# Performance work log

Hardware: AMD Instinct MI355X
Metric: run time of the kernel (lower is better)

## Reference

```python
import jax, jax.numpy as jnp
import numpy as np
import math

N_QUBITS = 10
N_VQC_LAYERS = 3
N_ACTIONS = 3
B = 4096
T = 128
D = 1 << N_QUBITS
IU, JU = np.triu_indices(N_QUBITS, 1)  # combinations(range(N),2) order


def _ry(a):
    # [B] (or scalar) -> [...,2,2] complex64 RY(a)
    c, s = jnp.cos(a * 0.5), jnp.sin(a * 0.5)
    return jnp.stack([jnp.stack([c, -s], -1), jnp.stack([s, c], -1)], -2).astype(jnp.complex64)


def _rz(a):
    h = a.astype(jnp.complex64) * 0.5
    z = jnp.zeros_like(h)
    return jnp.stack([jnp.stack([jnp.exp(-1j * h), z], -1), jnp.stack([z, jnp.exp(1j * h)], -1)], -2)


def _rot(w):
    # Rot(phi,theta,omega) = RZ(omega) @ RY(theta) @ RZ(phi); w=[phi,theta,omega]
    return _rz(w[2]) @ _ry(w[1]) @ _rz(w[0])


def _apply_1q(state, gate, q, n):
    # apply 2x2 gate to qubit q of [B, 2^n] state (bit q has stride 2^(n-q-1))
    b, d = state.shape
    lo = 1 << (n - q - 1)
    hi = 1 << q
    s = state.reshape(b, hi, 2, lo)
    if gate.ndim == 3:
        s = jnp.einsum('bij,bhjl->bhil', gate, s)
    else:
        s = jnp.einsum('ij,bhjl->bhil', gate, s)
    return s.reshape(b, d)


def _static_tables(n, n_layers):
    s = np.arange(1 << n)
    # IsingZZ sign masks: +1 if bits differ, -1 if equal (matches torch buffer)
    masks = np.stack([
        np.where(((s >> (n - 1 - qi)) & 1) ^ ((s >> (n - 1 - qj)) & 1) == 1, 1.0, -1.0)
        for qi, qj in zip(IU, JU)
    ]).astype(np.float32)
    # PauliZ expectation signs per qubit
    zsigns = np.where(((s[None, :] >> (n - 1 - np.arange(n)[:, None])) & 1) == 0, 1.0, -1.0).astype(np.float32)
    # CNOT ring as index permutations (same math as the dense matmul in torch)
    perms = []
    for l in range(n_layers):
        rng = l % (n - 1) + 1 if n > 1 else 1
        layer = []
        for ctrl in range(n):
            tgt = (ctrl + rng) % n
            cb = (s >> (n - 1 - ctrl)) & 1
            layer.append(np.where(cb == 1, s ^ (1 << (n - 1 - tgt)), s))
        perms.append(layer)
    return masks, zsigns, perms


MASKS, ZSIGNS, PERMS = _static_tables(N_QUBITS, N_VQC_LAYERS)


def setup_inputs() -> dict:
    key = jax.random.key(0)
    k1, k2, k3, k4 = jax.random.split(key, 4)
    return {
        'c_kt': jax.random.normal(k1, (B, T, N_QUBITS), jnp.float32),
        'delta_c_kt': jax.random.normal(k2, (B, T, N_QUBITS), jnp.float32),
        'vqc_weights': jax.random.normal(k3, (N_VQC_LAYERS, N_QUBITS, 3), jnp.float32),
        'w_proj': jax.random.normal(k4, (N_ACTIONS, N_QUBITS), jnp.float32) / math.sqrt(N_QUBITS),
        'b_proj': jnp.zeros((N_ACTIONS,), jnp.float32),
        'log_alpha': jnp.zeros((), jnp.float32),
    }


def reference(c_kt, delta_c_kt, vqc_weights, w_proj, b_proj, log_alpha):
    n, L = N_QUBITS, N_VQC_LAYERS
    b, t, k_ = c_kt.shape
    # --- IsingCouplingEstimator: Pearson corr -> tanh(rho * alpha), zero diag ---
    feat = c_kt + 0.5 * delta_c_kt
    X = jnp.swapaxes(feat, 1, 2)                      # [B, K, T]
    Xc = X - X.mean(-1, keepdims=True)
    std = jnp.maximum(jnp.sqrt((Xc * Xc).sum(-1, keepdims=True) / (t - 1)), 1e-8)
    Xn = Xc / std
    rho = jnp.einsum('bit,bjt->bij', Xn, Xn) / (t - 1)
    rho = rho * (1.0 - jnp.eye(k_, dtype=rho.dtype))
    J = jnp.tanh(rho * jnp.exp(log_alpha))            # [B, K, K]
    j_upper = J[:, IU, JU]                            # [B, K*(K-1)/2]

    # --- angle encoding from last timestep ---
    theta = c_kt[:, -1, :]                            # [B, K]
    phi = delta_c_kt[:, -1, :]

    # --- TorchVQC state-vector simulation ---
    state = jnp.zeros((b, D), jnp.complex64).at[:, 0].set(1.0 + 0j)
    for q in range(n):
        state = _apply_1q(state, _ry(theta[:, q]), q, n)
        state = _apply_1q(state, _rz(phi[:, q]), q, n)
    # all IsingZZ phases fused: exp(0.5j * pi * sum_p J_p * mask_p)
    ang = math.pi * (j_upper @ jnp.asarray(MASKS))    # [B, D]
    state = state * jnp.exp(0.5j * ang.astype(jnp.complex64))
    for l in range(L):
        for q in range(n):
            state = _apply_1q(state, _rot(vqc_weights[l, q]), q, n)
        for q in range(n):
            state = state[:, PERMS[l][q]]             # CNOT as permutation
        if l < L - 1:                                 # data re-uploading
            for q in range(n):
                state = _apply_1q(state, _ry(theta[:, q] * 0.5), q, n)
                state = _apply_1q(state, _rz(phi[:, q] * 0.5), q, n)
    probs = jnp.real(state) ** 2 + jnp.imag(state) ** 2
    expvals = probs @ jnp.asarray(ZSIGNS).T           # [B, N] <Z_k>

    # --- logit projection ---
    return expvals @ w_proj.T + b_proj                # [B, n_actions]
```

## Files before the change

### kernel.cpp

```cpp
#include <hip/hip_runtime.h>


typedef float v2 __attribute__((ext_vector_type(2)));

struct M10 { unsigned row[10]; };
constexpr M10 mident() { M10 m{}; for (int i=0;i<10;++i) m.row[i]=1u<<i; return m; }
constexpr M10 mmul(M10 A, M10 B) {
  M10 C{};
  for (int i=0;i<10;++i){ unsigned x=0; for (int j=0;j<10;++j) if ((A.row[i]>>j)&1u) x ^= B.row[j]; C.row[i]=x; }
  return C;
}
constexpr M10 cnotT(int ctrl, int rng) {
  const int tgt = (ctrl + rng) % 10;
  const int cb = 9 - ctrl, tb = 9 - tgt;
  M10 m = mident(); m.row[tb] = (1u<<tb)|(1u<<cb); return m;
}
constexpr M10 blockPinv(int rng) { M10 m = cnotT(0,rng); for (int c=1;c<10;++c) m = mmul(m, cnotT(c,rng)); return m; }
constexpr M10 blockP(int rng)    { M10 m = cnotT(9,rng); for (int c=8;c>=0;--c) m = mmul(m, cnotT(c,rng)); return m; }
constexpr unsigned mcol(M10 A, int c) { unsigned x=0; for (int i=0;i<10;++i) x |= ((A.row[i]>>c)&1u)<<i; return x; }
constexpr int par(unsigned x){ int p=0; for (int i=0;i<10;++i) p ^= (int)((x>>i)&1u); return p; }
constexpr int topbit4(int x){ int b=0; for (int i=1;i<4;++i) if (x>>i) b=i; return 1<<b; }

constexpr M10 Q1  = blockP(1);
constexpr M10 Q1i = blockPinv(1);
constexpr M10 Q2  = mmul(blockP(2), Q1);
constexpr M10 Q2i = mmul(Q1i, blockPinv(2));
constexpr M10 Q3  = mmul(blockP(3), Q2);

static_assert(mmul(Q1, Q1i).row[0]==1u && mmul(Q1,Q1i).row[9]==(1u<<9), "inv1");
static_assert(mmul(Q2, Q2i).row[0]==1u && mmul(Q2,Q2i).row[7]==(1u<<7), "inv2");
static_assert(par(mcol(Q1i,0)&Q1.row[0]) && par(mcol(Q1i,5)&Q1.row[5]) && par(mcol(Q1i,9)&Q1.row[9]), "dual1");
static_assert(par(mcol(Q2i,0)&Q2.row[0]) && par(mcol(Q2i,4)&Q2.row[4]) && par(mcol(Q2i,9)&Q2.row[9]), "dual2");

template<int CTRL>
__device__ __forceinline__ float dppf(float v) {
  return __int_as_float(__builtin_amdgcn_update_dpp(
      0, __float_as_int(v), CTRL, 0xF, 0xF, true));
}

template<int MASK>
__device__ __forceinline__ float xany(float v, int baddr) {
  constexpr int QC[4] = {0, 0xB1, 0x4E, 0x1B};
  if constexpr (MASK == 0) return v;
  else if constexpr (MASK <= 3) return dppf<QC[MASK]>(v);
  else if constexpr (MASK == 4) return dppf<0x141>(dppf<0x1B>(v));
  else if constexpr (MASK == 8) return dppf<0x128>(v);
  else if constexpr (MASK >= 9 && MASK <= 11) return dppf<QC[MASK&3]>(dppf<0x128>(v));
  else if constexpr (MASK < 32) return __int_as_float(__builtin_amdgcn_ds_swizzle(__float_as_int(v), (MASK<<10)|0x1F));
  else return __int_as_float(__builtin_amdgcn_ds_bpermute(baddr, __float_as_int(v)));
}
template<int MASK>
__device__ __forceinline__ v2 xany2(v2 v, int baddr) {
  v2 r; r.x = xany<MASK>(v.x, baddr); r.y = xany<MASK>(v.y, baddr); return r;
}

template<int LM>
__device__ __forceinline__ float xshfl(float v) {
  if constexpr (LM == 1) return dppf<0xB1>(v);
  else if constexpr (LM == 2) return dppf<0x4E>(v);
  else if constexpr (LM == 4) return dppf<0x141>(dppf<0x1B>(v));
  else if constexpr (LM == 8) return dppf<0x128>(v);
  else if constexpr (LM == 16) return __int_as_float(__builtin_amdgcn_ds_swizzle(__float_as_int(v), 0x401F));
  else return __shfl_xor(v, 32);
}

template<int B, int NP>
__device__ __forceinline__ void fstage(float* p, int lane) {
  #pragma unroll
  for (int i = 0; i < NP; ++i) {
    const float send = (lane & B) ? p[i] : p[i + NP];
    const float recv = xshfl<B>(send);
    const float keep = (lane & B) ? p[i + NP] : p[i];
    p[i] = keep + recv;
  }
}
constexpr int holder_lane45(int v) {
  const int a = v >= 24; int r = v - 24 * a;
  const int b = r >= 12; r -= 12 * b;
  const int c = r >= 6;  r -= 6 * c;
  const int d = r >= 3;  r -= 3 * d;
  const int e = r >= 2;  r -= 2 * e;
  return a | (b << 1) | (c << 2) | (d << 3) | (e << 4) | (r << 5);
}
constexpr int holder_lane10(int v) {
  const int a = v >= 5; int r = v - 5 * a;
  const int b = r >= 3; r -= 3 * b;
  const int c = r >= 2; r -= 2 * c;
  return a | (b << 1) | (c << 2) | (r << 3);
}

__device__ __forceinline__ float rfl(float x) {
  return __int_as_float(__builtin_amdgcn_readfirstlane(__float_as_int(x)));
}
#define RLg(g_, x_) __int_as_float(__builtin_amdgcn_readlane(__float_as_int(x_), (g_)))

__device__ __forceinline__ float fast_tanh(float x) {
  return 1.0f - 2.0f / (__expf(2.0f * x) + 1.0f);
}
__device__ __forceinline__ v2 sneg(v2 a) {
  v2 r; r.x = -a.y; r.y = a.x; return r;
}

template<int M, int V>
__device__ __forceinline__ void gate_g(v2 (&st)[16], int lane,
                                       float ar, float ai, float br, float bi) {
  constexpr int MR = M & 15, ML = (M >> 4) & 63;
  constexpr int VR = V & 15, VL = (V >> 4) & 63;
  bool hl = false;
  if constexpr (VL != 0) hl = (__builtin_popcount(lane & VL) & 1) != 0;
  const float aiX = hl ? -ai : ai;
  const float brX = hl ? -br : br;
  int baddr = 0;
  if constexpr (ML >= 32) baddr = (lane ^ ML) << 2;
  if constexpr (MR == 0) {
    #pragma unroll
    for (int r = 0; r < 16; ++r) {
      const v2 p = xany2<ML>(st[r], baddr);
      const v2 a = st[r];
      if ((__builtin_popcount(r & VR) & 1) == 0)
        st[r] = ar*a + aiX*sneg(a) + brX*p + bi*sneg(p);
      else
        st[r] = ar*a - aiX*sneg(a) - brX*p + bi*sneg(p);
    }
  } else {
    constexpr int HB = topbit4(MR);
    #pragma unroll
    for (int r = 0; r < 16; ++r) {
      if ((r & HB) == 0) {
        const int r1 = r ^ MR;
        v2 pa, pb;
        if constexpr (ML == 0) { pa = st[r1]; pb = st[r]; }
        else { pa = xany2<ML>(st[r1], baddr); pb = xany2<ML>(st[r], baddr); }
        const v2 a = st[r], b = st[r1];
        if ((__builtin_popcount(r & VR) & 1) == 0)
          st[r] = ar*a + aiX*sneg(a) + brX*pa + bi*sneg(pa);
        else
          st[r] = ar*a - aiX*sneg(a) - brX*pa + bi*sneg(pa);
        if ((__builtin_popcount(r1 & VR) & 1) == 0)
          st[r1] = ar*b + aiX*sneg(b) + brX*pb + bi*sneg(pb);
        else
          st[r1] = ar*b - aiX*sneg(b) - brX*pb + bi*sneg(pb);
      }
    }
  }
}

template<int I, int J>
__device__ __forceinline__ void pair_accum(float t, int lane, float& Cc,
                                           float (&dcf)[4], float (&ecf)[6]) {
  if constexpr (J <= 5) {
    const bool diff = (((lane >> (5 - I)) ^ (lane >> (5 - J))) & 1) != 0;
    Cc += diff ? -t : t;
  } else if constexpr (I <= 5) {
    const bool b = ((lane >> (5 - I)) & 1) != 0;
    dcf[J - 6] += b ? -t : t;
  } else {
    constexpr int eb = (I == 6) ? 0 : (I == 7) ? 3 : 5;
    ecf[eb + (J - I - 1)] = t;
  }
}
#define PACC(v_, i_, j_) pair_accum<i_, j_>(RLg(holder_lane45(v_), tl), lane, Cc, dcoef, ecoef);

#define GATE0(g_, q_) gate_g<(1<<(9-(q_))), (1<<(9-(q_)))>(st, lane, \
    RLg(g_,Mr00), RLg(g_,Mi00), RLg(g_,Mr01), RLg(g_,Mi01));
#define GATE1(g_, q_) gate_g<(int)mcol(Q1i,9-(q_)), (int)Q1.row[9-(q_)]>(st, lane, \
    RLg(g_,Mr00), RLg(g_,Mi00), RLg(g_,Mr01), RLg(g_,Mi01));
#define GATE2(g_, q_) gate_g<(int)mcol(Q2i,9-(q_)), (int)Q2.row[9-(q_)]>(st, lane, \
    RLg(g_,Mr00), RLg(g_,Mi00), RLg(g_,Mr01), RLg(g_,Mi01));

extern "C" __global__ void __launch_bounds__(256, 2)
qhl_kernel(const float* __restrict__ c_kt, const float* __restrict__ dc_kt,
           const float* __restrict__ vw,  const float* __restrict__ w_proj,
           const float* __restrict__ b_proj, const float* __restrict__ log_alpha,
           float* __restrict__ out) {
  const int wave = threadIdx.x >> 6;
  const int lane = threadIdx.x & 63;
  const int bid  = blockIdx.x * 4 + wave;

  const float* c   = c_kt  + (size_t)bid * 1280;
  const float* dcp = dc_kt + (size_t)bid * 1280;

  float Mr00, Mi00, Mr01, Mi01;
  {
    const int g = lane < 30 ? lane : 0;
    const int l = g / 10, q = g - l * 10;
    const float w0 = vw[g*3+0], w1 = vw[g*3+1], w2 = vw[g*3+2];
    float cY, sY; __sincosf(0.5f*w1, &sY, &cY);
    float ca, sa; __sincosf(0.5f*(w0+w2), &sa, &ca);
    float cb, sb; __sincosf(0.5f*(w0-w2), &sb, &cb);
    const float r00r =  cY*ca, r00i = -cY*sa, r01r = -sY*cb, r01i = -sY*sb;
    if (l == 0) {
      Mr00 = r00r; Mi00 = r00i; Mr01 = r01r; Mi01 = r01i;
    } else {
      const float thq = c[1270 + q], phq = dcp[1270 + q];
      float cy, sy; __sincosf(0.25f * thq, &sy, &cy);
      float cz, sz; __sincosf(0.25f * phq, &sz, &cz);
      const float e00r =  cy*cz, e00i = -cy*sz, e01r = -sy*cz, e01i =  sy*sz;
      const float e10r =  sy*cz, e10i =  sy*sz, e11r =  cy*cz, e11i =  cy*sz;
      Mr00 = r00r*e00r - r00i*e00i + r01r*e10r - r01i*e10i;
      Mi00 = r00r*e00i + r00i*e00r + r01r*e10i + r01i*e10r;
      Mr01 = r00r*e01r - r00i*e01i + r01r*e11r - r01i*e11i;
      Mi01 = r00r*e01i + r00i*e01r + r01r*e11i + r01i*e11r;
    }
  }

  v2 ym[10];
  {
    const float2* c0 = (const float2*)(c   + lane * 10);
    const float2* d0 = (const float2*)(dcp + lane * 10);
    const float2* c1 = (const float2*)(c   + (lane + 64) * 10);
    const float2* d1 = (const float2*)(dcp + (lane + 64) * 10);
    #pragma unroll
    for (int k = 0; k < 5; ++k) {
      const float2 a0 = c0[k], b0 = d0[k], a1 = c1[k], b1 = d1[k];
      ym[2*k].x   = a0.x + 0.5f * b0.x;  ym[2*k].y   = a1.x + 0.5f * b1.x;
      ym[2*k+1].x = a0.y + 0.5f * b0.y;  ym[2*k+1].y = a1.y + 0.5f * b1.y;
    }
  }

  {
    float mb[6];
    float m10a[10];
    #pragma unroll
    for (int k = 0; k < 10; ++k) m10a[k] = ym[k].x + ym[k].y;
    #pragma unroll
    for (int i = 0; i < 5; ++i) {
      const float send = (lane & 1) ? m10a[i] : m10a[i + 5];
      const float recv = xshfl<1>(send);
      const float keep = (lane & 1) ? m10a[i + 5] : m10a[i];
      mb[i] = keep + recv;
    }
    mb[5] = 0.0f;
    fstage<2, 3>(mb, lane);
    mb[3] = 0.0f;
    fstage<4, 2>(mb, lane);
    fstage<8, 1>(mb, lane);
    mb[0] += xshfl<16>(mb[0]);
    mb[0] += xshfl<32>(mb[0]);
    mb[0] *= (1.0f / 128.0f);
    #pragma unroll
    for (int k = 0; k < 10; ++k) {
      const float mk = RLg(holder_lane10(k), mb[0]);
      ym[k].x -= mk; ym[k].y -= mk;
    }
    float s10[10];
    #pragma unroll
    for (int k = 0; k < 10; ++k) { const v2 sq = ym[k] * ym[k]; s10[k] = sq.x + sq.y; }
    #pragma unroll
    for (int i = 0; i < 5; ++i) {
      const float send = (lane & 1) ? s10[i] : s10[i + 5];
      const float recv = xshfl<1>(send);
      const float keep = (lane & 1) ? s10[i + 5] : s10[i];
      mb[i] = keep + recv;
    }
    mb[5] = 0.0f;
    fstage<2, 3>(mb, lane);
    mb[3] = 0.0f;
    fstage<4, 2>(mb, lane);
    fstage<8, 1>(mb, lane);
    mb[0] += xshfl<16>(mb[0]);
    mb[0] += xshfl<32>(mb[0]);
    const float rsv = fminf(__builtin_amdgcn_rsqf(mb[0] * (1.0f / 127.0f)), 1e8f);
    #pragma unroll
    for (int k = 0; k < 10; ++k) {
      const float rk = RLg(holder_lane10(k), rsv);
      ym[k].x *= rk; ym[k].y *= rk;
    }
  }

  const float expA = rfl(__expf(log_alpha[0]));
  float Cc = 0.0f, dcoef[4] = {0, 0, 0, 0}, ecoef[6];
  float tl;
  {
    constexpr int PI_[45] = {0,0,0,0,0,0,0,0,0, 1,1,1,1,1,1,1,1, 2,2,2,2,2,2,2,
                             3,3,3,3,3,3, 4,4,4,4,4, 5,5,5,5, 6,6,6, 7,7, 8};
    constexpr int PJ_[45] = {1,2,3,4,5,6,7,8,9, 2,3,4,5,6,7,8,9, 3,4,5,6,7,8,9,
                             4,5,6,7,8,9, 5,6,7,8,9, 6,7,8,9, 7,8,9, 8,9, 9};
    float p[48];
    #pragma unroll
    for (int v = 0; v < 45; ++v) {
      const v2 pr = ym[PI_[v]] * ym[PJ_[v]];
      p[v] = pr.x + pr.y;
    }
    p[45] = 0.0f; p[46] = 0.0f; p[47] = 0.0f;
    fstage<1, 24>(p, lane);
    fstage<2, 12>(p, lane);
    fstage<4, 6>(p, lane);
    fstage<8, 3>(p, lane);
    p[3] = 0.0f;
    fstage<16, 2>(p, lane);
    fstage<32, 1>(p, lane);
    const float sc = expA * (1.0f / 127.0f);
    tl = -1.5707963267948966f * fast_tanh(p[0] * sc);
  }
  PACC(0,0,1) PACC(1,0,2) PACC(2,0,3) PACC(3,0,4) PACC(4,0,5) PACC(5,0,6) PACC(6,0,7) PACC(7,0,8) PACC(8,0,9)
  PACC(9,1,2) PACC(10,1,3) PACC(11,1,4) PACC(12,1,5) PACC(13,1,6) PACC(14,1,7) PACC(15,1,8) PACC(16,1,9)
  PACC(17,2,3) PACC(18,2,4) PACC(19,2,5) PACC(20,2,6) PACC(21,2,7) PACC(22,2,8) PACC(23,2,9)
  PACC(24,3,4) PACC(25,3,5) PACC(26,3,6) PACC(27,3,7) PACC(28,3,8) PACC(29,3,9)
  PACC(30,4,5) PACC(31,4,6) PACC(32,4,7) PACC(33,4,8) PACC(34,4,9)
  PACC(35,5,6) PACC(36,5,7) PACC(37,5,8) PACC(38,5,9)
  PACC(39,6,7) PACC(40,6,8) PACC(41,6,9)
  PACC(42,7,8) PACC(43,7,9)
  PACC(44,8,9)

  float th[10], ph[10];
  #pragma unroll
  for (int q = 0; q < 10; ++q) {
    th[q] = rfl(c[1270 + q]);
    ph[q] = rfl(dcp[1270 + q]);
  }

  float Rr_l, Ri_l;
  {
    const int rr = lane & 15;
    float prr = 1.0f, pri = 0.0f;
    #pragma unroll
    for (int t = 0; t < 4; ++t) {
      float cy, sy; __sincosf(0.5f * th[6 + t], &sy, &cy);
      float cz, sz; __sincosf(0.5f * ph[6 + t], &sz, &cz);
      const bool b = ((rr >> (3 - t)) & 1) != 0;
      const float fr = b ? sy * cz : cy * cz;
      const float fi = b ? sy * sz : -cy * sz;
      const float nr = prr * fr - pri * fi;
      pri = prr * fi + pri * fr;
      prr = nr;
    }
    Rr_l = prr; Ri_l = pri;
  }

  v2 st[16];
  {
    v2 L; L.x = 1.0f; L.y = 0.0f;
    #pragma unroll
    for (int q = 0; q < 6; ++q) {
      float cy, sy; __sincosf(0.5f * th[q], &sy, &cy);
      float cz, sz; __sincosf(0.5f * ph[q], &sz, &cz);
      const bool b = ((lane >> (5 - q)) & 1) != 0;
      const float zr = b ? sy * cz : cy * cz;
      const float zi = b ? sy * sz : -cy * sz;
      L = zr * L + zi * sneg(L);
    }
    #pragma unroll
    for (int r = 0; r < 16; ++r) {
      const int b3 = (r >> 3) & 1, b2 = (r >> 2) & 1, b1 = (r >> 1) & 1, b0 = r & 1;
      const float Rr = RLg(r, Rr_l);
      const float Ri = RLg(r, Ri_l);
      float h = Cc;
      h += b3 ? -dcoef[0] : dcoef[0];
      h += b2 ? -dcoef[1] : dcoef[1];
      h += b1 ? -dcoef[2] : dcoef[2];
      h += b0 ? -dcoef[3] : dcoef[3];
      h += (b3 ^ b2) ? -ecoef[0] : ecoef[0];
      h += (b3 ^ b1) ? -ecoef[1] : ecoef[1];
      h += (b3 ^ b0) ? -ecoef[2] : ecoef[2];
      h += (b2 ^ b1) ? -ecoef[3] : ecoef[3];
      h += (b2 ^ b0) ? -ecoef[4] : ecoef[4];
      h += (b1 ^ b0) ? -ecoef[5] : ecoef[5];
      float sn, cs; __sincosf(h, &sn, &cs);
      const v2 p = cs * L + sn * sneg(L);
      st[r] = Rr * p + Ri * sneg(p);
    }
  }

  GATE0(0,0) GATE0(1,1) GATE0(2,2) GATE0(3,3) GATE0(4,4)
  GATE0(5,5) GATE0(6,6) GATE0(7,7) GATE0(8,8) GATE0(9,9)
  GATE1(10,0) GATE1(11,1) GATE1(12,2) GATE1(13,3) GATE1(14,4)
  GATE1(15,5) GATE1(16,6) GATE1(17,7) GATE1(18,8) GATE1(19,9)
  GATE2(20,0) GATE2(21,1) GATE2(22,2) GATE2(23,3) GATE2(24,4)
  GATE2(25,5) GATE2(26,6) GATE2(27,7) GATE2(28,8) GATE2(29,9)

  float e[10] = {0,0,0,0,0,0,0,0,0,0};
  #pragma unroll
  for (int r = 0; r < 16; ++r) {
    const v2 sq = st[r] * st[r];
    const float pp = sq.x + sq.y;
    #pragma unroll
    for (int q = 0; q < 10; ++q) {
      const bool s = (__builtin_popcount(r & (int)(Q3.row[9-q] & 15u)) & 1) != 0;
      e[q] += s ? -pp : pp;
    }
  }
  float mv[10];
  #pragma unroll
  for (int q = 0; q < 10; ++q) {
    const int wl = (int)((Q3.row[9-q] >> 4) & 63u);
    const bool sl = wl ? ((__builtin_popcount(lane & wl) & 1) != 0) : false;
    mv[q] = sl ? -e[q] : e[q];
  }
  {
    float fb[6];
    #pragma unroll
    for (int i = 0; i < 5; ++i) {
      const float send = (lane & 1) ? mv[i] : mv[i + 5];
      const float recv = xshfl<1>(send);
      const float keep = (lane & 1) ? mv[i + 5] : mv[i];
      fb[i] = keep + recv;
    }
    fb[5] = 0.0f;
    fstage<2, 3>(fb, lane);
    fb[3] = 0.0f;
    fstage<4, 2>(fb, lane);
    fstage<8, 1>(fb, lane);
    fb[0] += xshfl<16>(fb[0]);
    fb[0] += xshfl<32>(fb[0]);
    float ev[10];
    #pragma unroll
    for (int k = 0; k < 10; ++k) ev[k] = RLg(holder_lane10(k), fb[0]);
    if (lane < 3) {
      float acc = b_proj[lane];
      #pragma unroll
      for (int i = 0; i < 10; ++i) acc += w_proj[lane * 10 + i] * ev[i];
      out[(size_t)bid * 3 + lane] = acc;
    }
  }
}

extern "C" void kernel_launch(void* const* d_in, const int* in_sizes, int n_in,
                              void* d_out, int out_size, void* d_ws, size_t ws_size,
                              hipStream_t stream) {
  (void)in_sizes; (void)n_in; (void)d_ws; (void)ws_size; (void)out_size;
  const float* c_kt      = (const float*)d_in[0];
  const float* dc_kt     = (const float*)d_in[1];
  const float* vw        = (const float*)d_in[2];
  const float* w_proj    = (const float*)d_in[3];
  const float* b_proj    = (const float*)d_in[4];
  const float* log_alpha = (const float*)d_in[5];
  float* out = (float*)d_out;
  qhl_kernel<<<dim3(1024), dim3(256), 0, stream>>>(c_kt, dc_kt, vw, w_proj,
                                                   b_proj, log_alpha, out);
}
```

Before: 126.6 us.

## Split each sample's state vector across two waves with LDS exchange

Each batch element now runs on a 128-thread block (two waves) instead of one wave, so every thread holds 8 amplitudes instead of 16 and loads one time step instead of two. Qubit bit 9 becomes the wave index, and gates that touch it swap amplitudes through shared memory between two block barriers. Cross-wave sums for the statistics and the final expectations also go through LDS. The goal is lower register pressure and more parallelism per sample, at the cost of extra barriers and LDS traffic on the cross-wave gates.

```diff
diff --git a/kernel.cpp b/kernel.cpp
--- a/kernel.cpp
+++ b/kernel.cpp
@@ -19,14 +19,13 @@
 constexpr M10 blockP(int rng)    { M10 m = cnotT(9,rng); for (int c=8;c>=0;--c) m = mmul(m, cnotT(c,rng)); return m; }
 constexpr unsigned mcol(M10 A, int c) { unsigned x=0; for (int i=0;i<10;++i) x |= ((A.row[i]>>c)&1u)<<i; return x; }
 constexpr int par(unsigned x){ int p=0; for (int i=0;i<10;++i) p ^= (int)((x>>i)&1u); return p; }
-constexpr int topbit4(int x){ int b=0; for (int i=1;i<4;++i) if (x>>i) b=i; return 1<<b; }
+constexpr int topbit3(int x){ int b=0; for (int i=1;i<3;++i) if (x>>i) b=i; return 1<<b; }
 
 constexpr M10 Q1  = blockP(1);
 constexpr M10 Q1i = blockPinv(1);
 constexpr M10 Q2  = mmul(blockP(2), Q1);
 constexpr M10 Q2i = mmul(Q1i, blockPinv(2));
 constexpr M10 Q3  = mmul(blockP(3), Q2);
-
 static_assert(mmul(Q1, Q1i).row[0]==1u && mmul(Q1,Q1i).row[9]==(1u<<9), "inv1");
 static_assert(mmul(Q2, Q2i).row[0]==1u && mmul(Q2,Q2i).row[7]==(1u<<7), "inv2");
 static_assert(par(mcol(Q1i,0)&Q1.row[0]) && par(mcol(Q1i,5)&Q1.row[5]) && par(mcol(Q1i,9)&Q1.row[9]), "dual1");
@@ -37,7 +36,6 @@
   return __int_as_float(__builtin_amdgcn_update_dpp(
       0, __float_as_int(v), CTRL, 0xF, 0xF, true));
 }
-
 template<int MASK>
 __device__ __forceinline__ float xany(float v, int baddr) {
   constexpr int QC[4] = {0, 0xB1, 0x4E, 0x1B};
@@ -53,7 +51,6 @@
 __device__ __forceinline__ v2 xany2(v2 v, int baddr) {
   v2 r; r.x = xany<MASK>(v.x, baddr); r.y = xany<MASK>(v.y, baddr); return r;
 }
-
 template<int LM>
 __device__ __forceinline__ float xshfl(float v) {
   if constexpr (LM == 1) return dppf<0xB1>(v);
@@ -63,7 +60,6 @@
   else if constexpr (LM == 16) return __int_as_float(__builtin_amdgcn_ds_swizzle(__float_as_int(v), 0x401F));
   else return __shfl_xor(v, 32);
 }
-
 template<int B, int NP>
 __device__ __forceinline__ void fstage(float* p, int lane) {
   #pragma unroll
@@ -97,24 +93,40 @@
 __device__ __forceinline__ float fast_tanh(float x) {
   return 1.0f - 2.0f / (__expf(2.0f * x) + 1.0f);
 }
-__device__ __forceinline__ v2 sneg(v2 a) {
-  v2 r; r.x = -a.y; r.y = a.x; return r;
-}
+__device__ __forceinline__ v2 sneg(v2 a) { v2 r; r.x = -a.y; r.y = a.x; return r; }
 
 template<int M, int V>
-__device__ __forceinline__ void gate_g(v2 (&st)[16], int lane,
+__device__ __forceinline__ void gate_g(v2 (&st)[8], int lane, int sidx, float2* xb,
                                        float ar, float ai, float br, float bi) {
-  constexpr int MR = M & 15, ML = (M >> 4) & 63;
-  constexpr int VR = V & 15, VL = (V >> 4) & 63;
+  constexpr int MW = (M >> 9) & 1, ML = (M >> 3) & 63, MR = M & 7;
+  constexpr int VC = (((V >> 9) & 1) << 6) | ((V >> 3) & 63);
+  constexpr int VR = V & 7;
   bool hl = false;
-  if constexpr (VL != 0) hl = (__builtin_popcount(lane & VL) & 1) != 0;
+  if constexpr (VC != 0) hl = (__builtin_popcount(sidx & VC) & 1) != 0;
   const float aiX = hl ? -ai : ai;
   const float brX = hl ? -br : br;
-  int baddr = 0;
-  if constexpr (ML >= 32) baddr = (lane ^ ML) << 2;
-  if constexpr (MR == 0) {
-    #pragma unroll
-    for (int r = 0; r < 16; ++r) {
+  if constexpr (MW == 1) {
+    #pragma unroll
+    for (int r = 0; r < 8; ++r) { float2 t; t.x = st[r].x; t.y = st[r].y; xb[r*128 + sidx] = t; }
+    __syncthreads();
+    const int ptid = sidx ^ (64 | ML);
+    v2 p[8];
+    #pragma unroll
+    for (int r = 0; r < 8; ++r) { const float2 t = xb[(r^MR)*128 + ptid]; p[r].x = t.x; p[r].y = t.y; }
+    #pragma unroll
+    for (int r = 0; r < 8; ++r) {
+      const v2 a = st[r];
+      if ((__builtin_popcount(r & VR) & 1) == 0)
+        st[r] = ar*a + aiX*sneg(a) + brX*p[r] + bi*sneg(p[r]);
+      else
+        st[r] = ar*a - aiX*sneg(a) - brX*p[r] + bi*sneg(p[r]);
+    }
+    __syncthreads();
+  } else if constexpr (MR == 0) {
+    int baddr = 0;
+    if constexpr (ML >= 32) baddr = (lane ^ ML) << 2;
+    #pragma unroll
+    for (int r = 0; r < 8; ++r) {
       const v2 p = xany2<ML>(st[r], baddr);
       const v2 a = st[r];
       if ((__builtin_popcount(r & VR) & 1) == 0)
@@ -123,9 +135,11 @@
         st[r] = ar*a - aiX*sneg(a) - brX*p + bi*sneg(p);
     }
   } else {
-    constexpr int HB = topbit4(MR);
-    #pragma unroll
-    for (int r = 0; r < 16; ++r) {
+    constexpr int HB = topbit3(MR);
+    int baddr = 0;
+    if constexpr (ML >= 32) baddr = (lane ^ ML) << 2;
+    #pragma unroll
+    for (int r = 0; r < 8; ++r) {
       if ((r & HB) == 0) {
         const int r1 = r ^ MR;
         v2 pa, pb;
@@ -146,36 +160,40 @@
 }
 
 template<int I, int J>
-__device__ __forceinline__ void pair_accum(float t, int lane, float& Cc,
-                                           float (&dcf)[4], float (&ecf)[6]) {
-  if constexpr (J <= 5) {
-    const bool diff = (((lane >> (5 - I)) ^ (lane >> (5 - J))) & 1) != 0;
+__device__ __forceinline__ void pair_accum(float t, int sidx, float& Cc,
+                                           float (&dcf)[3], float (&ecf)[3]) {
+  if constexpr (J <= 6) {
+    const bool diff = (((sidx >> (6 - I)) ^ (sidx >> (6 - J))) & 1) != 0;
     Cc += diff ? -t : t;
-  } else if constexpr (I <= 5) {
-    const bool b = ((lane >> (5 - I)) & 1) != 0;
-    dcf[J - 6] += b ? -t : t;
+  } else if constexpr (I <= 6) {
+    const bool b = ((sidx >> (6 - I)) & 1) != 0;
+    dcf[J - 7] += b ? -t : t;
   } else {
-    constexpr int eb = (I == 6) ? 0 : (I == 7) ? 3 : 5;
-    ecf[eb + (J - I - 1)] = t;
-  }
-}
-#define PACC(v_, i_, j_) pair_accum<i_, j_>(RLg(holder_lane45(v_), tl), lane, Cc, dcoef, ecoef);
-
-#define GATE0(g_, q_) gate_g<(1<<(9-(q_))), (1<<(9-(q_)))>(st, lane, \
+    constexpr int eb = (I == 7) ? (J - 8) : 2;
+    ecf[eb] = t;
+  }
+}
+#define PACC(v_, i_, j_) pair_accum<i_, j_>(RLg(holder_lane45(v_), tl), sidx, Cc, dcoef, ecoef);
+
+#define GATE0(g_, q_) gate_g<(1<<(9-(q_))), (1<<(9-(q_)))>(st, lane, sidx, xb, \
     RLg(g_,Mr00), RLg(g_,Mi00), RLg(g_,Mr01), RLg(g_,Mi01));
-#define GATE1(g_, q_) gate_g<(int)mcol(Q1i,9-(q_)), (int)Q1.row[9-(q_)]>(st, lane, \
+#define GATE1(g_, q_) gate_g<(int)mcol(Q1i,9-(q_)), (int)Q1.row[9-(q_)]>(st, lane, sidx, xb, \
     RLg(g_,Mr00), RLg(g_,Mi00), RLg(g_,Mr01), RLg(g_,Mi01));
-#define GATE2(g_, q_) gate_g<(int)mcol(Q2i,9-(q_)), (int)Q2.row[9-(q_)]>(st, lane, \
+#define GATE2(g_, q_) gate_g<(int)mcol(Q2i,9-(q_)), (int)Q2.row[9-(q_)]>(st, lane, sidx, xb, \
     RLg(g_,Mr00), RLg(g_,Mi00), RLg(g_,Mr01), RLg(g_,Mi01));
 
-extern "C" __global__ void __launch_bounds__(256, 2)
+extern "C" __global__ void __launch_bounds__(128, 8)
 qhl_kernel(const float* __restrict__ c_kt, const float* __restrict__ dc_kt,
            const float* __restrict__ vw,  const float* __restrict__ w_proj,
            const float* __restrict__ b_proj, const float* __restrict__ log_alpha,
            float* __restrict__ out) {
-  const int wave = threadIdx.x >> 6;
-  const int lane = threadIdx.x & 63;
-  const int bid  = blockIdx.x * 4 + wave;
+  __shared__ float2 xbuf[8 * 128];
+  float2* xb = xbuf;
+  float*  fb = (float*)xbuf;
+
+  const int sidx = threadIdx.x;
+  const int lane = sidx & 63;
+  const int bid  = blockIdx.x;
 
   const float* c   = c_kt  + (size_t)bid * 1280;
   const float* dcp = dc_kt + (size_t)bid * 1280;
@@ -204,30 +222,25 @@
     }
   }
 
-  v2 ym[10];
-  {
-    const float2* c0 = (const float2*)(c   + lane * 10);
-    const float2* d0 = (const float2*)(dcp + lane * 10);
-    const float2* c1 = (const float2*)(c   + (lane + 64) * 10);
-    const float2* d1 = (const float2*)(dcp + (lane + 64) * 10);
+  float y[10];
+  {
+    const float2* c0 = (const float2*)(c   + sidx * 10);
+    const float2* d0 = (const float2*)(dcp + sidx * 10);
     #pragma unroll
     for (int k = 0; k < 5; ++k) {
-      const float2 a0 = c0[k], b0 = d0[k], a1 = c1[k], b1 = d1[k];
-      ym[2*k].x   = a0.x + 0.5f * b0.x;  ym[2*k].y   = a1.x + 0.5f * b1.x;
-      ym[2*k+1].x = a0.y + 0.5f * b0.y;  ym[2*k+1].y = a1.y + 0.5f * b1.y;
+      const float2 a0 = c0[k], b0 = d0[k];
+      y[2*k]   = a0.x + 0.5f * b0.x;
+      y[2*k+1] = a0.y + 0.5f * b0.y;
     }
   }
 
   {
     float mb[6];
-    float m10a[10];
-    #pragma unroll
-    for (int k = 0; k < 10; ++k) m10a[k] = ym[k].x + ym[k].y;
     #pragma unroll
     for (int i = 0; i < 5; ++i) {
-      const float send = (lane & 1) ? m10a[i] : m10a[i + 5];
+      const float send = (lane & 1) ? y[i] : y[i + 5];
       const float recv = xshfl<1>(send);
-      const float keep = (lane & 1) ? m10a[i + 5] : m10a[i];
+      const float keep = (lane & 1) ? y[i + 5] : y[i];
       mb[i] = keep + recv;
     }
     mb[5] = 0.0f;
@@ -237,15 +250,14 @@
     fstage<8, 1>(mb, lane);
     mb[0] += xshfl<16>(mb[0]);
     mb[0] += xshfl<32>(mb[0]);
-    mb[0] *= (1.0f / 128.0f);
-    #pragma unroll
-    for (int k = 0; k < 10; ++k) {
-      const float mk = RLg(holder_lane10(k), mb[0]);
-      ym[k].x -= mk; ym[k].y -= mk;
-    }
+    fb[sidx] = mb[0]; __syncthreads();
+    mb[0] = (mb[0] + fb[sidx ^ 64]) * (1.0f / 128.0f); __syncthreads();
+    #pragma unroll
+    for (int k = 0; k < 10; ++k) y[k] -= RLg(holder_lane10(k), mb[0]);
+
     float s10[10];
     #pragma unroll
-    for (int k = 0; k < 10; ++k) { const v2 sq = ym[k] * ym[k]; s10[k] = sq.x + sq.y; }
+    for (int k = 0; k < 10; ++k) s10[k] = y[k] * y[k];
     #pragma unroll
     for (int i = 0; i < 5; ++i) {
       const float send = (lane & 1) ? s10[i] : s10[i + 5];
@@ -260,16 +272,15 @@
     fstage<8, 1>(mb, lane);
     mb[0] += xshfl<16>(mb[0]);
     mb[0] += xshfl<32>(mb[0]);
+    fb[sidx] = mb[0]; __syncthreads();
+    mb[0] += fb[sidx ^ 64]; __syncthreads();
     const float rsv = fminf(__builtin_amdgcn_rsqf(mb[0] * (1.0f / 127.0f)), 1e8f);
     #pragma unroll
-    for (int k = 0; k < 10; ++k) {
-      const float rk = RLg(holder_lane10(k), rsv);
-      ym[k].x *= rk; ym[k].y *= rk;
-    }
+    for (int k = 0; k < 10; ++k) y[k] *= RLg(holder_lane10(k), rsv);
   }
 
   const float expA = rfl(__expf(log_alpha[0]));
-  float Cc = 0.0f, dcoef[4] = {0, 0, 0, 0}, ecoef[6];
+  float Cc = 0.0f, dcoef[3] = {0, 0, 0}, ecoef[3];
   float tl;
   {
     constexpr int PI_[45] = {0,0,0,0,0,0,0,0,0, 1,1,1,1,1,1,1,1, 2,2,2,2,2,2,2,
@@ -278,10 +289,7 @@
                              4,5,6,7,8,9, 5,6,7,8,9, 6,7,8,9, 7,8,9, 8,9, 9};
     float p[48];
     #pragma unroll
-    for (int v = 0; v < 45; ++v) {
-      const v2 pr = ym[PI_[v]] * ym[PJ_[v]];
-      p[v] = pr.x + pr.y;
-    }
+    for (int v = 0; v < 45; ++v) p[v] = y[PI_[v]] * y[PJ_[v]];
     p[45] = 0.0f; p[46] = 0.0f; p[47] = 0.0f;
     fstage<1, 24>(p, lane);
     fstage<2, 12>(p, lane);
@@ -290,8 +298,9 @@
     p[3] = 0.0f;
     fstage<16, 2>(p, lane);
     fstage<32, 1>(p, lane);
-    const float sc = expA * (1.0f / 127.0f);
-    tl = -1.5707963267948966f * fast_tanh(p[0] * sc);
+    fb[sidx] = p[0]; __syncthreads();
+    p[0] += fb[sidx ^ 64]; __syncthreads();
+    tl = -1.5707963267948966f * fast_tanh(p[0] * (expA * (1.0f / 127.0f)));
   }
   PACC(0,0,1) PACC(1,0,2) PACC(2,0,3) PACC(3,0,4) PACC(4,0,5) PACC(5,0,6) PACC(6,0,7) PACC(7,0,8) PACC(8,0,9)
   PACC(9,1,2) PACC(10,1,3) PACC(11,1,4) PACC(12,1,5) PACC(13,1,6) PACC(14,1,7) PACC(15,1,8) PACC(16,1,9)
@@ -312,13 +321,13 @@
 
   float Rr_l, Ri_l;
   {
-    const int rr = lane & 15;
+    const int rr = lane & 7;
     float prr = 1.0f, pri = 0.0f;
     #pragma unroll
-    for (int t = 0; t < 4; ++t) {
-      float cy, sy; __sincosf(0.5f * th[6 + t], &sy, &cy);
-      float cz, sz; __sincosf(0.5f * ph[6 + t], &sz, &cz);
-      const bool b = ((rr >> (3 - t)) & 1) != 0;
+    for (int t = 0; t < 3; ++t) {
+      float cy, sy; __sincosf(0.5f * th[7 + t], &sy, &cy);
+      float cz, sz; __sincosf(0.5f * ph[7 + t], &sz, &cz);
+      const bool b = ((rr >> (2 - t)) & 1) != 0;
       const float fr = b ? sy * cz : cy * cz;
       const float fi = b ? sy * sz : -cy * sz;
       const float nr = prr * fr - pri * fi;
@@ -328,34 +337,30 @@
     Rr_l = prr; Ri_l = pri;
   }
 
-  v2 st[16];
+  v2 st[8];
   {
     v2 L; L.x = 1.0f; L.y = 0.0f;
     #pragma unroll
-    for (int q = 0; q < 6; ++q) {
+    for (int q = 0; q < 7; ++q) {
       float cy, sy; __sincosf(0.5f * th[q], &sy, &cy);
       float cz, sz; __sincosf(0.5f * ph[q], &sz, &cz);
-      const bool b = ((lane >> (5 - q)) & 1) != 0;
+      const bool b = ((sidx >> (6 - q)) & 1) != 0;
       const float zr = b ? sy * cz : cy * cz;
       const float zi = b ? sy * sz : -cy * sz;
       L = zr * L + zi * sneg(L);
     }
     #pragma unroll
-    for (int r = 0; r < 16; ++r) {
-      const int b3 = (r >> 3) & 1, b2 = (r >> 2) & 1, b1 = (r >> 1) & 1, b0 = r & 1;
+    for (int r = 0; r < 8; ++r) {
+      const int b2 = (r >> 2) & 1, b1 = (r >> 1) & 1, b0 = r & 1;
       const float Rr = RLg(r, Rr_l);
       const float Ri = RLg(r, Ri_l);
       float h = Cc;
-      h += b3 ? -dcoef[0] : dcoef[0];
-      h += b2 ? -dcoef[1] : dcoef[1];
-      h += b1 ? -dcoef[2] : dcoef[2];
-      h += b0 ? -dcoef[3] : dcoef[3];
-      h += (b3 ^ b2) ? -ecoef[0] : ecoef[0];
-      h += (b3 ^ b1) ? -ecoef[1] : ecoef[1];
-      h += (b3 ^ b0) ? -ecoef[2] : ecoef[2];
-      h += (b2 ^ b1) ? -ecoef[3] : ecoef[3];
-      h += (b2 ^ b0) ? -ecoef[4] : ecoef[4];
-      h += (b1 ^ b0) ? -ecoef[5] : ecoef[5];
+      h += b2 ? -dcoef[0] : dcoef[0];
+      h += b1 ? -dcoef[1] : dcoef[1];
+      h += b0 ? -dcoef[2] : dcoef[2];
+      h += (b2 ^ b1) ? -ecoef[0] : ecoef[0];
+      h += (b2 ^ b0) ? -ecoef[1] : ecoef[1];
+      h += (b1 ^ b0) ? -ecoef[2] : ecoef[2];
       float sn, cs; __sincosf(h, &sn, &cs);
       const v2 p = cs * L + sn * sneg(L);
       st[r] = Rr * p + Ri * sneg(p);
@@ -371,46 +376,48 @@
 
   float e[10] = {0,0,0,0,0,0,0,0,0,0};
   #pragma unroll
-  for (int r = 0; r < 16; ++r) {
+  for (int r = 0; r < 8; ++r) {
     const v2 sq = st[r] * st[r];
     const float pp = sq.x + sq.y;
     #pragma unroll
     for (int q = 0; q < 10; ++q) {
-      const bool s = (__builtin_popcount(r & (int)(Q3.row[9-q] & 15u)) & 1) != 0;
+      const bool s = (__builtin_popcount(r & (int)(Q3.row[9-q] & 7u)) & 1) != 0;
       e[q] += s ? -pp : pp;
     }
   }
   float mv[10];
   #pragma unroll
   for (int q = 0; q < 10; ++q) {
-    const int wl = (int)((Q3.row[9-q] >> 4) & 63u);
-    const bool sl = wl ? ((__builtin_popcount(lane & wl) & 1) != 0) : false;
+    const int wl = (int)((((Q3.row[9-q] >> 9) & 1u) << 6) | ((Q3.row[9-q] >> 3) & 63u));
+    const bool sl = wl ? ((__builtin_popcount(sidx & wl) & 1) != 0) : false;
     mv[q] = sl ? -e[q] : e[q];
   }
   {
-    float fb[6];
+    float fbv[6];
     #pragma unroll
     for (int i = 0; i < 5; ++i) {
       const float send = (lane & 1) ? mv[i] : mv[i + 5];
       const float recv = xshfl<1>(send);
       const float keep = (lane & 1) ? mv[i + 5] : mv[i];
-      fb[i] = keep + recv;
-    }
-    fb[5] = 0.0f;
-    fstage<2, 3>(fb, lane);
-    fb[3] = 0.0f;
-    fstage<4, 2>(fb, lane);
-    fstage<8, 1>(fb, lane);
-    fb[0] += xshfl<16>(fb[0]);
-    fb[0] += xshfl<32>(fb[0]);
+      fbv[i] = keep + recv;
+    }
+    fbv[5] = 0.0f;
+    fstage<2, 3>(fbv, lane);
+    fbv[3] = 0.0f;
+    fstage<4, 2>(fbv, lane);
+    fstage<8, 1>(fbv, lane);
+    fbv[0] += xshfl<16>(fbv[0]);
+    fbv[0] += xshfl<32>(fbv[0]);
+    fb[sidx] = fbv[0]; __syncthreads();
+    fbv[0] += fb[sidx ^ 64];
     float ev[10];
     #pragma unroll
-    for (int k = 0; k < 10; ++k) ev[k] = RLg(holder_lane10(k), fb[0]);
-    if (lane < 3) {
-      float acc = b_proj[lane];
+    for (int k = 0; k < 10; ++k) ev[k] = RLg(holder_lane10(k), fbv[0]);
+    if (sidx < 3) {
+      float acc = b_proj[sidx];
       #pragma unroll
-      for (int i = 0; i < 10; ++i) acc += w_proj[lane * 10 + i] * ev[i];
-      out[(size_t)bid * 3 + lane] = acc;
+      for (int i = 0; i < 10; ++i) acc += w_proj[sidx * 10 + i] * ev[i];
+      out[(size_t)bid * 3 + sidx] = acc;
     }
   }
 }
@@ -426,6 +433,6 @@
   const float* b_proj    = (const float*)d_in[4];
   const float* log_alpha = (const float*)d_in[5];
   float* out = (float*)d_out;
-  qhl_kernel<<<dim3(1024), dim3(256), 0, stream>>>(c_kt, dc_kt, vw, w_proj,
+  qhl_kernel<<<dim3(4096), dim3(128), 0, stream>>>(c_kt, dc_kt, vw, w_proj,
                                                    b_proj, log_alpha, out);
 }
```

After: 133.1 us. 5.1% more time.
